# Optimization experiments

Measured on AMD Instinct MI355X. Metric: run time of the kernel, lower is better.

## Reference

```python
import jax, jax.numpy as jnp
import numpy as np

WINDOW_SIZE = 11
SIGMA = 1.5
C1 = 0.01 ** 2
C2 = 0.03 ** 2


def _gaussian_window(window_size, sigma, channel):
    x = np.arange(window_size)
    g = np.exp(-((x - window_size // 2) ** 2) / (2.0 * sigma ** 2))
    g = g / g.sum()
    w2d = np.outer(g, g).astype(np.float32)  # [K,K]
    # depthwise kernel [C,1,K,K] (OIHW with feature_group_count=C)
    return jnp.asarray(np.broadcast_to(w2d, (channel, 1, window_size, window_size)))


def _depthwise_conv(x, window):
    # x: [B,C,H,W], window: [C,1,K,K]; SAME padding, groups=C
    pad = WINDOW_SIZE // 2
    return jax.lax.conv_general_dilated(
        x, window,
        window_strides=(1, 1),
        padding=[(pad, pad), (pad, pad)],
        dimension_numbers=('NCHW', 'OIHW', 'NCHW'),
        feature_group_count=x.shape[1],
    )


def setup_inputs() -> dict:
    key = jax.random.key(0)
    k1, k2 = jax.random.split(key)
    shape = (16, 3, 512, 512)
    img1 = jax.random.uniform(k1, shape, dtype=jnp.float32)
    img2 = jax.random.uniform(k2, shape, dtype=jnp.float32)
    return {"img1": img1, "img2": img2}


def reference(img1, img2):
    channel = img1.shape[1]
    window = _gaussian_window(WINDOW_SIZE, SIGMA, channel).astype(img1.dtype)

    mu1 = _depthwise_conv(img1, window)
    mu2 = _depthwise_conv(img2, window)
    mu1_sq = mu1 * mu1
    mu2_sq = mu2 * mu2
    mu1_mu2 = mu1 * mu2

    sigma1_sq = _depthwise_conv(img1 * img1, window) - mu1_sq
    sigma2_sq = _depthwise_conv(img2 * img2, window) - mu2_sq
    sigma12 = _depthwise_conv(img1 * img2, window) - mu1_mu2

    ssim_map = ((2 * mu1_mu2 + C1) * (2 * sigma12 + C2)) / (
        (mu1_sq + mu2_sq + C1) * (sigma1_sq + sigma2_sq + C2))
    # size_average=True -> scalar mean
    return jnp.mean(ssim_map)
```

## Files before the change

### kernel.cpp

```cpp
#include <hip/hip_runtime.h>

#define IMG 512
#define NPLANES 48
#define TW 64
#define TH 32
#define RD 5
#define KW 11
#define VC (TW + 2*RD)
#define WPAD 80
#define NTX (IMG/TW)
#define NTY (IMG/TH)
#define TPP (NTX*NTY)
#define NBLOCKS (NPLANES*TPP)
#define NPIX (16.0f*3.0f*512.0f*512.0f)

__device__ __forceinline__ float fast_rcp(float d) {
    float r = __builtin_amdgcn_rcpf(d);
    r = r * (2.0f - d * r);
    return r;
}

__global__ __launch_bounds__(256) void ssim_kernel(
    const float* __restrict__ img1, const float* __restrict__ img2,
    float* __restrict__ partial)
{
    __shared__ float v[5][TH][WPAD];
    __shared__ float wsum[4];

    const float cw[KW] = {
        0.00102838f, 0.00759876f, 0.03600077f, 0.10936069f, 0.21300553f,
        0.26601172f,
        0.21300553f, 0.10936069f, 0.03600077f, 0.00759876f, 0.00102838f
    };

    const int tid = threadIdx.x;
    const int blk = blockIdx.x;
    const int plane = blk / TPP;
    const int t     = blk % TPP;
    const int ty0 = (t / NTX) * TH;
    const int tx0 = (t % NTX) * TW;
    const float* __restrict__ p1 = img1 + (size_t)plane * IMG * IMG;
    const float* __restrict__ p2 = img2 + (size_t)plane * IMG * IMG;

    for (int task = tid; task < VC * 4; task += 256) {
        const int col = task % VC;
        const int seg = task / VC;
        const int gx  = tx0 + col - RD;
        const bool xok = (gx >= 0) && (gx < IMG);
        const int r0 = seg * 8;

        float a[18], b[18];
        #pragma unroll
        for (int k = 0; k < 18; k++) {
            const int gy = ty0 + r0 + k - RD;
            const bool ok = xok && (gy >= 0) && (gy < IMG);
            const int gi = gy * IMG + gx;
            a[k] = ok ? p1[gi] : 0.f;
            b[k] = ok ? p2[gi] : 0.f;
        }

        #pragma unroll
        for (int k = 0; k < 8; k++) {
            float sa = 0.f, sb = 0.f, saa = 0.f, sbb = 0.f, sab = 0.f;
            #pragma unroll
            for (int d = 0; d < KW; d++) {
                const float wv = cw[d];
                const float av = a[k + d];
                const float bv = b[k + d];
                const float wa = wv * av;
                const float wb = wv * bv;
                sa  += wa;
                sb  += wb;
                saa += wa * av;
                sbb += wb * bv;
                sab += wa * bv;
            }
            const int r = r0 + k;
            v[0][r][col] = sa;
            v[1][r][col] = sb;
            v[2][r][col] = saa;
            v[3][r][col] = sbb;
            v[4][r][col] = sab;
        }
    }
    __syncthreads();

    const float C1 = 1e-4f;
    const float C2 = 9e-4f;
    float acc = 0.f;
    #pragma unroll
    for (int it = 0; it < 2; it++) {
        const int task = tid + it * 256;
        const int j = task & 15;
        const int r = task >> 4;
        float res[5][4];
        #pragma unroll
        for (int arr = 0; arr < 5; arr++) {
            const float4* row = (const float4*)&v[arr][r][0];
            const float4 q0 = row[j + 0];
            const float4 q1 = row[j + 1];
            const float4 q2 = row[j + 2];
            const float4 q3 = row[j + 3];
            const float vals[16] = {
                q0.x, q0.y, q0.z, q0.w,
                q1.x, q1.y, q1.z, q1.w,
                q2.x, q2.y, q2.z, q2.w,
                q3.x, q3.y, q3.z, q3.w
            };
            #pragma unroll
            for (int o = 0; o < 4; o++) {
                float s = 0.f;
                #pragma unroll
                for (int d = 0; d < KW; d++)
                    s += cw[d] * vals[o + d];
                res[arr][o] = s;
            }
        }
        #pragma unroll
        for (int o = 0; o < 4; o++) {
            const float mu1 = res[0][o];
            const float mu2 = res[1][o];
            const float x11 = res[2][o];
            const float x22 = res[3][o];
            const float x12 = res[4][o];
            const float mu1s = mu1 * mu1;
            const float mu2s = mu2 * mu2;
            const float mu12 = mu1 * mu2;
            const float s1  = x11 - mu1s;
            const float s2  = x22 - mu2s;
            const float s12 = x12 - mu12;
            const float num = (2.f * mu12 + C1) * (2.f * s12 + C2);
            const float den = (mu1s + mu2s + C1) * (s1 + s2 + C2);
            acc += num * fast_rcp(den);
        }
    }

    #pragma unroll
    for (int off = 32; off > 0; off >>= 1)
        acc += __shfl_down(acc, off, 64);
    const int lane = tid & 63;
    const int wv_i = tid >> 6;
    if (lane == 0) wsum[wv_i] = acc;
    __syncthreads();
    if (tid == 0)
        partial[blk] = (wsum[0] + wsum[1]) + (wsum[2] + wsum[3]);
}

__global__ __launch_bounds__(256) void ssim_reduce_kernel(
    const float* __restrict__ partial, float* __restrict__ out)
{
    float acc = 0.f;
    for (int i = threadIdx.x; i < NBLOCKS; i += 256)
        acc += partial[i];
    #pragma unroll
    for (int off = 32; off > 0; off >>= 1)
        acc += __shfl_down(acc, off, 64);
    __shared__ float wsum[4];
    const int lane = threadIdx.x & 63;
    const int wv_i = threadIdx.x >> 6;
    if (lane == 0) wsum[wv_i] = acc;
    __syncthreads();
    if (threadIdx.x == 0)
        out[0] = ((wsum[0] + wsum[1]) + (wsum[2] + wsum[3])) * (1.0f / NPIX);
}

extern "C" void kernel_launch(void* const* d_in, const int* in_sizes, int n_in,
                              void* d_out, int out_size, void* d_ws, size_t ws_size,
                              hipStream_t stream) {
    const float* img1 = (const float*)d_in[0];
    const float* img2 = (const float*)d_in[1];
    float* out = (float*)d_out;
    float* partial = (float*)d_ws;

    ssim_kernel<<<NBLOCKS, 256, 0, stream>>>(img1, img2, partial);
    ssim_reduce_kernel<<<1, 256, 0, stream>>>(partial, out);
}
```

Before: 164.5 us.

## Restructure SSIM vertical pass, use symmetric taps, fuse reduction via atomics

Several changes at once. The vertical pass now scatters each loaded sample into 8 output accumulators, computing products once per input instead of once per tap. Interior tiles skip bounds checks. The horizontal pass uses symmetric-weight folding and a narrower final LDS read. The shared-memory row pad changes from 80 to 84 and occupancy is hinted with launch_bounds(256,3). The separate reduce kernel is replaced by per-block atomicAdd into the output after a memset, which removes a launch but adds atomic contention and a nondeterministic summation order.

```diff
diff --git a/kernel.cpp b/kernel.cpp
--- a/kernel.cpp
+++ b/kernel.cpp
@@ -7,7 +7,7 @@
 #define RD 5
 #define KW 11
 #define VC (TW + 2*RD)
-#define WPAD 80
+#define WPAD 84
 #define NTX (IMG/TW)
 #define NTY (IMG/TH)
 #define TPP (NTX*NTY)
@@ -20,9 +20,16 @@
     return r;
 }
 
-__global__ __launch_bounds__(256) void ssim_kernel(
+__device__ __forceinline__ float tap11(float x0, float x1, float x2, float x3,
+                                       float x4, float x5, float x6, float x7,
+                                       float x8, float x9, float x10) {
+    return 0.00102838f*(x0+x10) + 0.00759876f*(x1+x9) + 0.03600077f*(x2+x8)
+         + 0.10936069f*(x3+x7) + 0.21300553f*(x4+x6) + 0.26601172f*x5;
+}
+
+__global__ __launch_bounds__(256, 3) void ssim_kernel(
     const float* __restrict__ img1, const float* __restrict__ img2,
-    float* __restrict__ partial)
+    float* __restrict__ out)
 {
     __shared__ float v[5][TH][WPAD];
     __shared__ float wsum[4];
@@ -42,45 +49,71 @@
     const float* __restrict__ p1 = img1 + (size_t)plane * IMG * IMG;
     const float* __restrict__ p2 = img2 + (size_t)plane * IMG * IMG;
 
+    const bool interior = (tx0 != 0) && (tx0 != IMG - TW) &&
+                          (ty0 != 0) && (ty0 != IMG - TH);
+
     for (int task = tid; task < VC * 4; task += 256) {
         const int col = task % VC;
         const int seg = task / VC;
         const int gx  = tx0 + col - RD;
-        const bool xok = (gx >= 0) && (gx < IMG);
-        const int r0 = seg * 8;
+        const int r0  = seg * 8;
+        const int gy0 = ty0 + r0 - RD;
 
         float a[18], b[18];
+        if (interior) {
+            const float* __restrict__ pa = p1 + (size_t)gy0 * IMG + gx;
+            const float* __restrict__ pb = p2 + (size_t)gy0 * IMG + gx;
+            #pragma unroll
+            for (int k = 0; k < 18; k++) {
+                a[k] = pa[k * IMG];
+                b[k] = pb[k * IMG];
+            }
+        } else {
+            const bool xok = (gx >= 0) && (gx < IMG);
+            #pragma unroll
+            for (int k = 0; k < 18; k++) {
+                const int gy = gy0 + k;
+                const bool ok = xok && (gy >= 0) && (gy < IMG);
+                const int gi = gy * IMG + gx;
+                a[k] = ok ? p1[gi] : 0.f;
+                b[k] = ok ? p2[gi] : 0.f;
+            }
+        }
+
+        float s[8][5];
+        #pragma unroll
+        for (int o = 0; o < 8; o++)
+            #pragma unroll
+            for (int q = 0; q < 5; q++)
+                s[o][q] = 0.f;
+
         #pragma unroll
         for (int k = 0; k < 18; k++) {
-            const int gy = ty0 + r0 + k - RD;
-            const bool ok = xok && (gy >= 0) && (gy < IMG);
-            const int gi = gy * IMG + gx;
-            a[k] = ok ? p1[gi] : 0.f;
-            b[k] = ok ? p2[gi] : 0.f;
+            const float av = a[k], bv = b[k];
+            const float aa = av * av;
+            const float bb = bv * bv;
+            const float ab = av * bv;
+            const int olo = (k - 10 < 0) ? 0 : k - 10;
+            const int ohi = (k < 7) ? k : 7;
+            #pragma unroll
+            for (int o = olo; o <= ohi; o++) {
+                const float w = cw[k - o];
+                s[o][0] += w * av;
+                s[o][1] += w * bv;
+                s[o][2] += w * aa;
+                s[o][3] += w * bb;
+                s[o][4] += w * ab;
+            }
         }
 
         #pragma unroll
-        for (int k = 0; k < 8; k++) {
-            float sa = 0.f, sb = 0.f, saa = 0.f, sbb = 0.f, sab = 0.f;
-            #pragma unroll
-            for (int d = 0; d < KW; d++) {
-                const float wv = cw[d];
-                const float av = a[k + d];
-                const float bv = b[k + d];
-                const float wa = wv * av;
-                const float wb = wv * bv;
-                sa  += wa;
-                sb  += wb;
-                saa += wa * av;
-                sbb += wb * bv;
-                sab += wa * bv;
-            }
-            const int r = r0 + k;
-            v[0][r][col] = sa;
-            v[1][r][col] = sb;
-            v[2][r][col] = saa;
-            v[3][r][col] = sbb;
-            v[4][r][col] = sab;
+        for (int o = 0; o < 8; o++) {
+            const int r = r0 + o;
+            v[0][r][col] = s[o][0];
+            v[1][r][col] = s[o][1];
+            v[2][r][col] = s[o][2];
+            v[3][r][col] = s[o][3];
+            v[4][r][col] = s[o][4];
         }
     }
     __syncthreads();
@@ -96,25 +129,16 @@
         float res[5][4];
         #pragma unroll
         for (int arr = 0; arr < 5; arr++) {
-            const float4* row = (const float4*)&v[arr][r][0];
+            const float4* row  = (const float4*)&v[arr][r][0];
+            const float2* row2 = (const float2*)row;
             const float4 q0 = row[j + 0];
             const float4 q1 = row[j + 1];
             const float4 q2 = row[j + 2];
-            const float4 q3 = row[j + 3];
-            const float vals[16] = {
-                q0.x, q0.y, q0.z, q0.w,
-                q1.x, q1.y, q1.z, q1.w,
-                q2.x, q2.y, q2.z, q2.w,
-                q3.x, q3.y, q3.z, q3.w
-            };
-            #pragma unroll
-            for (int o = 0; o < 4; o++) {
-                float s = 0.f;
-                #pragma unroll
-                for (int d = 0; d < KW; d++)
-                    s += cw[d] * vals[o + d];
-                res[arr][o] = s;
-            }
+            const float2 q3 = row2[2*(j + 3)];
+            res[arr][0] = tap11(q0.x,q0.y,q0.z,q0.w,q1.x,q1.y,q1.z,q1.w,q2.x,q2.y,q2.z);
+            res[arr][1] = tap11(q0.y,q0.z,q0.w,q1.x,q1.y,q1.z,q1.w,q2.x,q2.y,q2.z,q2.w);
+            res[arr][2] = tap11(q0.z,q0.w,q1.x,q1.y,q1.z,q1.w,q2.x,q2.y,q2.z,q2.w,q3.x);
+            res[arr][3] = tap11(q0.w,q1.x,q1.y,q1.z,q1.w,q2.x,q2.y,q2.z,q2.w,q3.x,q3.y);
         }
         #pragma unroll
         for (int o = 0; o < 4; o++) {
@@ -142,26 +166,10 @@
     const int wv_i = tid >> 6;
     if (lane == 0) wsum[wv_i] = acc;
     __syncthreads();
-    if (tid == 0)
-        partial[blk] = (wsum[0] + wsum[1]) + (wsum[2] + wsum[3]);
-}
-
-__global__ __launch_bounds__(256) void ssim_reduce_kernel(
-    const float* __restrict__ partial, float* __restrict__ out)
-{
-    float acc = 0.f;
-    for (int i = threadIdx.x; i < NBLOCKS; i += 256)
-        acc += partial[i];
-    #pragma unroll
-    for (int off = 32; off > 0; off >>= 1)
-        acc += __shfl_down(acc, off, 64);
-    __shared__ float wsum[4];
-    const int lane = threadIdx.x & 63;
-    const int wv_i = threadIdx.x >> 6;
-    if (lane == 0) wsum[wv_i] = acc;
-    __syncthreads();
-    if (threadIdx.x == 0)
-        out[0] = ((wsum[0] + wsum[1]) + (wsum[2] + wsum[3])) * (1.0f / NPIX);
+    if (tid == 0) {
+        const float total = (wsum[0] + wsum[1]) + (wsum[2] + wsum[3]);
+        atomicAdd(out, total * (1.0f / NPIX));
+    }
 }
 
 extern "C" void kernel_launch(void* const* d_in, const int* in_sizes, int n_in,
@@ -170,8 +178,7 @@
     const float* img1 = (const float*)d_in[0];
     const float* img2 = (const float*)d_in[1];
     float* out = (float*)d_out;
-    float* partial = (float*)d_ws;
 
-    ssim_kernel<<<NBLOCKS, 256, 0, stream>>>(img1, img2, partial);
-    ssim_reduce_kernel<<<1, 256, 0, stream>>>(partial, out);
+    hipMemsetAsync(out, 0, sizeof(float), stream);
+    ssim_kernel<<<NBLOCKS, 256, 0, stream>>>(img1, img2, out);
 }
```

Result: slower. 189.6 us (+15.3%).
